# Performance work log

Measured on AMD Instinct MI355X. Metric: run time of the kernel, lower is better.

## Reference

```python
import jax, jax.numpy as jnp
import numpy as np

B, L, C, OUT = 32, 1024, 64, 64
BN_EPS = 1e-5  # PyTorch BatchNorm1d default


def setup_inputs() -> dict:
    key = jax.random.key(0)
    kH, kA, kW = jax.random.split(key, 3)
    H = jax.random.normal(kH, (B, L, C), dtype=jnp.float32)
    A = jax.random.uniform(kA, (B, L, L), dtype=jnp.float32)  # positive degrees
    gamma = jnp.ones((C,), jnp.float32)
    beta = jnp.zeros((C,), jnp.float32)
    W = jax.random.normal(kW, (C, OUT), dtype=jnp.float32) * 0.05
    b = jnp.zeros((OUT,), jnp.float32)
    return {"H": H, "A": A, "gamma": gamma, "beta": beta, "W": W, "b": b}


def reference(H, A, gamma, beta, W, b):
    batch, l, c = H.shape
    # BatchNorm1d in train mode over the flattened (batch*l, c) node axis,
    # biased variance as in PyTorch.
    Hf = H.reshape(batch * l, c)
    mean = Hf.mean(axis=0)
    var = jnp.mean((Hf - mean) ** 2, axis=0)
    Hn = ((Hf - mean) * jax.lax.rsqrt(var + BN_EPS) * gamma + beta).reshape(batch, l, c)
    # Degree normalization: diag(d^0.5) @ A @ diag(d^-0.5) done as row/col scaling
    # (same math as the original's dense diagonal matmuls).
    d = A.sum(axis=2)                                   # [batch, l]
    A_norm = jnp.sqrt(d)[:, :, None] * A * jax.lax.rsqrt(d)[:, None, :]
    A_hat = jnp.eye(l, dtype=A.dtype) - A_norm          # I - D^0.5 A D^-0.5
    # Linear then batched propagation, LeakyReLU (default slope 0.01).
    X = Hn @ W + b                                      # [batch, l, out]
    out = jnp.einsum('bij,bjo->bio', A_hat, X)
    return jax.nn.leaky_relu(out, negative_slope=0.01)
```

## Files before the change

### kernel.cpp

```cpp
#include <hip/hip_runtime.h>

#define NB 32
#define NL 1024
#define NC 64
#define NO 64
constexpr float BN_EPS = 1e-5f;

#define D_OFF 128
#define PART_OFF 32896
#define YT_OFF 131072
#define ABF_OFF 2097152

typedef short          s16x8 __attribute__((ext_vector_type(8)));
typedef unsigned short u16x8 __attribute__((ext_vector_type(8)));
typedef unsigned short u16x4 __attribute__((ext_vector_type(4)));
typedef float          f32x16 __attribute__((ext_vector_type(16)));
typedef float          f32x4  __attribute__((ext_vector_type(4)));

__device__ inline unsigned short f2bf(float f) {
    union { float f; unsigned u; } v; v.f = f;
    unsigned u = v.u + 0x7FFFu + ((v.u >> 16) & 1u);
    return (unsigned short)(u >> 16);
}

__device__ inline void gload16(const void* g, void* l) {
    __builtin_amdgcn_global_load_lds(
        (const __attribute__((address_space(1))) unsigned int*)g,
        (__attribute__((address_space(3))) unsigned int*)l, 16, 0, 0);
}

__global__ __launch_bounds__(256) void degcvt_bn(
    const float* __restrict__ A, const float* __restrict__ H,
    float* __restrict__ ws, unsigned short* __restrict__ Abf) {
    __shared__ f32x4 smem4[2048];
    const int t = threadIdx.x;
    if (blockIdx.x < 1024) {
        const int lane = t & 63, w = t >> 6;
        const size_t row0 = (size_t)blockIdx.x * 32;
        const char* src  = (const char*)A   + row0 * 4096;
        char*       dstA = (char*)Abf       + row0 * 2048;
        const int lo = w * 4096 + lane * 16;
#define STG(bi, c) do {                                                        \
            char* d0 = (char*)(smem4 + (bi) * 1024) + lo;                      \
            const char* s0 = src + (c) * 16384 + lo;                           \
            gload16(s0,        d0);                                            \
            gload16(s0 + 1024, d0 + 1024);                                     \
            gload16(s0 + 2048, d0 + 2048);                                     \
            gload16(s0 + 3072, d0 + 3072);                                     \
        } while (0)
        STG(0, 0);
        __syncthreads();
#pragma unroll 1
        for (int c = 0; c < 8; ++c) {
            if (c + 1 < 8) STG((c + 1) & 1, c + 1);
            const char* cb = (const char*)(smem4 + (c & 1) * 1024) + lo;
            float s = 0.f;
            char* orow = dstA + (size_t)(c * 4 + w) * 2048 + lane * 8;
#pragma unroll
            for (int j = 0; j < 4; ++j) {
                f32x4 v = *(const f32x4*)(cb + j * 1024);
                u16x4 h;
                h[0] = f2bf(v.x); h[1] = f2bf(v.y);
                h[2] = f2bf(v.z); h[3] = f2bf(v.w);
                *(u16x4*)(orow + j * 512) = h;
                s += v.x + v.y + v.z + v.w;
            }
#pragma unroll
            for (int m = 32; m; m >>= 1) s += __shfl_xor(s, m, 64);
            if (lane == 0) ws[D_OFF + row0 + c * 4 + w] = s;
            __syncthreads();
        }
#undef STG
    } else {
        const int bb = blockIdx.x - 1024;
        const float4* Hv = (const float4*)H + bb * 4096;
        float s0 = 0.f, s1 = 0.f, s2 = 0.f, s3 = 0.f;
        float q0 = 0.f, q1 = 0.f, q2 = 0.f, q3 = 0.f;
#pragma unroll 4
        for (int s = 0; s < 16; ++s) {
            float4 v = Hv[s * 256 + t];
            s0 += v.x; q0 += v.x * v.x;
            s1 += v.y; q1 += v.y * v.y;
            s2 += v.z; q2 += v.z * v.z;
            s3 += v.w; q3 += v.w * v.w;
        }
        float* part = (float*)smem4;
        part[t * 8 + 0] = s0; part[t * 8 + 1] = s1;
        part[t * 8 + 2] = s2; part[t * 8 + 3] = s3;
        part[t * 8 + 4] = q0; part[t * 8 + 5] = q1;
        part[t * 8 + 6] = q2; part[t * 8 + 7] = q3;
        __syncthreads();
        if (t < 64) {
            const int g = t >> 2, e = t & 3;
            float a = 0.f, a2 = 0.f;
#pragma unroll
            for (int k = 0; k < 16; ++k) {
                a  += part[(g + 16 * k) * 8 + e];
                a2 += part[(g + 16 * k) * 8 + 4 + e];
            }
            ws[PART_OFF + bb * 64 + t] = a;
            ws[PART_OFF + 128 * 64 + bb * 64 + t] = a2;
        }
    }
}

__global__ __launch_bounds__(256) void linear_xy(
    const float* __restrict__ H, const float* __restrict__ Wm,
    const float* __restrict__ bias, const float* __restrict__ gamma,
    const float* __restrict__ beta, const float* __restrict__ ws,
    float* __restrict__ X, unsigned short* __restrict__ Yt) {
    __shared__ float Wl[NC * NO];
    __shared__ float hnbuf[4][NC];
    __shared__ unsigned short ytile[64][66];
    __shared__ float ls[256], ls2[256];
    __shared__ float sscale[64], sshift[64];
    const int b = blockIdx.x >> 4, ch = blockIdx.x & 15;
    const int r0g = b * NL + ch * 64;
    const int t = threadIdx.x, lane = t & 63, w = t >> 6;
    {
        const float* ps  = ws + PART_OFF;
        const float* ps2 = ws + PART_OFF + 128 * 64;
        const int c = t & 63, q = t >> 6;
        float s = 0.f, s2 = 0.f;
        for (int p = q * 32; p < q * 32 + 32; ++p) {
            s  += ps[p * 64 + c];
            s2 += ps2[p * 64 + c];
        }
        ls[t] = s; ls2[t] = s2;
        __syncthreads();
        if (t < 64) {
            float T  = ls[c]  + ls[c + 64]  + ls[c + 128]  + ls[c + 192];
            float T2 = ls2[c] + ls2[c + 64] + ls2[c + 128] + ls2[c + 192];
            const float n = (float)(NB * NL);
            float mean = T / n;
            float var  = T2 / n - mean * mean;
            float sc = gamma[c] * rsqrtf(var + BN_EPS);
            sscale[c] = sc;
            sshift[c] = beta[c] - mean * sc;
        }
    }
    for (int k = t; k < NC * NO; k += 256) Wl[k] = Wm[k];
    __syncthreads();
    const float sc = sscale[lane];
    const float sh = sshift[lane];
    const float bo = bias[lane];
    const float* dbuf = ws + D_OFF;
    for (int rr = w; rr < 64; rr += 4) {
        const int row = r0g + rr;
        float h = H[(size_t)row * NC + lane];
        hnbuf[w][lane] = h * sc + sh;
        float x = bo;
#pragma unroll
        for (int c4 = 0; c4 < NC; c4 += 4) {
            float4 h4 = *(const float4*)(&hnbuf[w][c4]);
            x += h4.x * Wl[(c4 + 0) * NO + lane];
            x += h4.y * Wl[(c4 + 1) * NO + lane];
            x += h4.z * Wl[(c4 + 2) * NO + lane];
            x += h4.w * Wl[(c4 + 3) * NO + lane];
        }
        X[(size_t)row * NO + lane] = x;
        ytile[rr][lane] = f2bf(x * rsqrtf(dbuf[row]));
    }
    __syncthreads();
    char* ybase = (char*)Yt + (size_t)(b * 16 + ch) * 8192;
#pragma unroll
    for (int i2 = 0; i2 < 16; ++i2) {
        const int col = i2 * 4 + w;
        *(unsigned short*)(ybase + ((col * 128 + lane * 2) ^ ((col & 7) << 4))) =
            ytile[lane][col];
    }
}

__global__ __launch_bounds__(256) void prop_mfma(
    const unsigned short* __restrict__ Abf, const unsigned short* __restrict__ Yt,
    const float* __restrict__ dbuf, float* __restrict__ XO) {

    __shared__ unsigned short Abuf[2][64 * 64];
    __shared__ unsigned short Ybuf[2][64 * 64];
    __shared__ float sdl[64];

    const int b  = blockIdx.x >> 4;
    const int mt = blockIdx.x & 15;
    const int i0 = mt * 64;
    const char* YbT = (const char*)Yt + (size_t)b * 16 * 8192;

    const int t    = threadIdx.x;
    const int lane = t & 63;
    const int w    = t >> 6;

    if (t < 64) sdl[t] = sqrtf(dbuf[b * NL + i0 + t]);

    const int L0  = w * 2048 + lane * 16;
    const int L1  = L0 + 1024;
    const int ar0 = L0 >> 7, ar1 = L1 >> 7;
    const char* Asrc0 = (const char*)Abf
        + ((size_t)(b * NL + i0 + ar0)) * 2048 + ((L0 & 127) ^ ((ar0 & 7) << 4));
    const char* Asrc1 = (const char*)Abf
        + ((size_t)(b * NL + i0 + ar1)) * 2048 + ((L1 & 127) ^ ((ar1 & 7) << 4));

    const int wr0  = (w >> 1) * 32;
    const int wc0  = (w & 1) * 32;
    const int frow = wr0 + (lane & 31);
    const int fcol = wc0 + (lane & 31);
    const int khb  = (lane >> 5) * 16;

    f32x16 acc;
#pragma unroll
    for (int r = 0; r < 16; ++r) acc[r] = 0.f;

#define STAGE(bi, kt) do {                                                     \
        char* adst = (char*)Abuf[bi];                                          \
        gload16(Asrc0 + (size_t)(kt) * 128, adst + L0);                        \
        gload16(Asrc1 + (size_t)(kt) * 128, adst + L1);                        \
        const char* ysrc = YbT + (size_t)(kt) * 8192;                          \
        char* ydst = (char*)Ybuf[bi];                                          \
        gload16(ysrc + L0, ydst + L0);                                         \
        gload16(ysrc + L1, ydst + L1);                                         \
    } while (0)

    STAGE(0, 0);
    __syncthreads();

#pragma unroll 1
    for (int kti = 0; kti < 16; ++kti) {
        const int nxt = kti + 1;
        if (nxt < 16) STAGE(nxt & 1, nxt);
        const char* ab  = (const char*)Abuf[kti & 1];
        const char* yb2 = (const char*)Ybuf[kti & 1];
#pragma unroll
        for (int ks = 0; ks < 4; ++ks) {
            const int kb = ks * 32 + khb;
            s16x8 af = *(const s16x8*)(ab  + ((frow * 128 + kb) ^ ((frow & 7) << 4)));
            s16x8 bf = *(const s16x8*)(yb2 + ((fcol * 128 + kb) ^ ((fcol & 7) << 4)));
            acc = __builtin_amdgcn_mfma_f32_32x32x16_bf16(af, bf, acc, 0, 0, 0);
        }
        __syncthreads();
    }
#undef STAGE

#pragma unroll
    for (int reg = 0; reg < 16; ++reg) {
        int row = (reg & 3) + 8 * (reg >> 2) + 4 * (lane >> 5);
        int i   = i0 + wr0 + row;
        int col = wc0 + (lane & 31);
        size_t idx = ((size_t)(b * NL + i)) * NO + col;
        float x = XO[idx];
        float v = x - sdl[wr0 + row] * acc[reg];
        XO[idx] = v > 0.f ? v : 0.01f * v;
    }
}

extern "C" void kernel_launch(void* const* d_in, const int* in_sizes, int n_in,
                              void* d_out, int out_size, void* d_ws, size_t ws_size,
                              hipStream_t stream) {
    const float* H     = (const float*)d_in[0];
    const float* A     = (const float*)d_in[1];
    const float* gamma = (const float*)d_in[2];
    const float* beta  = (const float*)d_in[3];
    const float* Wm    = (const float*)d_in[4];
    const float* bias  = (const float*)d_in[5];
    float* out = (float*)d_out;
    float* ws  = (float*)d_ws;
    unsigned short* Yt  = (unsigned short*)(ws + YT_OFF);
    unsigned short* Abf = (unsigned short*)(ws + ABF_OFF);

    degcvt_bn<<<1152, 256, 0, stream>>>(A, H, ws, Abf);
    linear_xy<<<512, 256, 0, stream>>>(H, Wm, bias, gamma, beta, ws, out, Yt);
    prop_mfma<<<512, 256, 0, stream>>>(Abf, Yt, ws + D_OFF, out);
}
```

Measured before the change: 69.94 us.

## Drop bf16 copy of A; convert fp32 A to bf16 inside propagation kernel

Removes the bf16 staging copy of the adjacency matrix written by the degree kernel. The propagation kernel now streams fp32 A tiles into LDS and packs them to bf16 with v_cvt_pk_bf16_f32 just before each MFMA. This avoids a large global write and the later bf16 read. In exchange it reads twice as many bytes of A in the matmul, doubles LDS for the A buffers, and adds conversion work in the inner loop.

```diff
diff --git a/kernel.cpp b/kernel.cpp
--- a/kernel.cpp
+++ b/kernel.cpp
@@ -9,11 +9,8 @@
 #define D_OFF 128
 #define PART_OFF 32896
 #define YT_OFF 131072
-#define ABF_OFF 2097152
 
 typedef short          s16x8 __attribute__((ext_vector_type(8)));
-typedef unsigned short u16x8 __attribute__((ext_vector_type(8)));
-typedef unsigned short u16x4 __attribute__((ext_vector_type(4)));
 typedef float          f32x16 __attribute__((ext_vector_type(16)));
 typedef float          f32x4  __attribute__((ext_vector_type(4)));
 
@@ -29,16 +26,24 @@
         (__attribute__((address_space(3))) unsigned int*)l, 16, 0, 0);
 }
 
-__global__ __launch_bounds__(256) void degcvt_bn(
+__device__ inline s16x8 cvt8(f32x4 lo, f32x4 hi) {
+    union { unsigned int i[4]; s16x8 v; } u;
+    asm("v_cvt_pk_bf16_f32 %0, %1, %2" : "=v"(u.i[0]) : "v"(lo.x), "v"(lo.y));
+    asm("v_cvt_pk_bf16_f32 %0, %1, %2" : "=v"(u.i[1]) : "v"(lo.z), "v"(lo.w));
+    asm("v_cvt_pk_bf16_f32 %0, %1, %2" : "=v"(u.i[2]) : "v"(hi.x), "v"(hi.y));
+    asm("v_cvt_pk_bf16_f32 %0, %1, %2" : "=v"(u.i[3]) : "v"(hi.z), "v"(hi.w));
+    return u.v;
+}
+
+__global__ __launch_bounds__(256) void deg_bn(
     const float* __restrict__ A, const float* __restrict__ H,
-    float* __restrict__ ws, unsigned short* __restrict__ Abf) {
+    float* __restrict__ ws) {
     __shared__ f32x4 smem4[2048];
     const int t = threadIdx.x;
     if (blockIdx.x < 1024) {
         const int lane = t & 63, w = t >> 6;
         const size_t row0 = (size_t)blockIdx.x * 32;
-        const char* src  = (const char*)A   + row0 * 4096;
-        char*       dstA = (char*)Abf       + row0 * 2048;
+        const char* src = (const char*)A + row0 * 4096;
         const int lo = w * 4096 + lane * 16;
 #define STG(bi, c) do {                                                        \
             char* d0 = (char*)(smem4 + (bi) * 1024) + lo;                      \
@@ -55,14 +60,9 @@
             if (c + 1 < 8) STG((c + 1) & 1, c + 1);
             const char* cb = (const char*)(smem4 + (c & 1) * 1024) + lo;
             float s = 0.f;
-            char* orow = dstA + (size_t)(c * 4 + w) * 2048 + lane * 8;
 #pragma unroll
             for (int j = 0; j < 4; ++j) {
                 f32x4 v = *(const f32x4*)(cb + j * 1024);
-                u16x4 h;
-                h[0] = f2bf(v.x); h[1] = f2bf(v.y);
-                h[2] = f2bf(v.z); h[3] = f2bf(v.w);
-                *(u16x4*)(orow + j * 512) = h;
                 s += v.x + v.y + v.z + v.w;
             }
 #pragma unroll
@@ -172,17 +172,18 @@
 }
 
 __global__ __launch_bounds__(256) void prop_mfma(
-    const unsigned short* __restrict__ Abf, const unsigned short* __restrict__ Yt,
+    const float* __restrict__ A, const unsigned short* __restrict__ Yt,
     const float* __restrict__ dbuf, float* __restrict__ XO) {
 
-    __shared__ unsigned short Abuf[2][64 * 64];
+    __shared__ float Abuf[2][64 * 64];
     __shared__ unsigned short Ybuf[2][64 * 64];
     __shared__ float sdl[64];
 
     const int b  = blockIdx.x >> 4;
     const int mt = blockIdx.x & 15;
     const int i0 = mt * 64;
-    const char* YbT = (const char*)Yt + (size_t)b * 16 * 8192;
+    const char* Abase = (const char*)A + ((size_t)(b * NL + i0)) * 4096;
+    const char* YbT   = (const char*)Yt + (size_t)b * 16 * 8192;
 
     const int t    = threadIdx.x;
     const int lane = t & 63;
@@ -190,32 +191,39 @@
 
     if (t < 64) sdl[t] = sqrtf(dbuf[b * NL + i0 + t]);
 
-    const int L0  = w * 2048 + lane * 16;
-    const int L1  = L0 + 1024;
-    const int ar0 = L0 >> 7, ar1 = L1 >> 7;
-    const char* Asrc0 = (const char*)Abf
-        + ((size_t)(b * NL + i0 + ar0)) * 2048 + ((L0 & 127) ^ ((ar0 & 7) << 4));
-    const char* Asrc1 = (const char*)Abf
-        + ((size_t)(b * NL + i0 + ar1)) * 2048 + ((L1 & 127) ^ ((ar1 & 7) << 4));
+    const int tr = t >> 4;
+    const int tc = (t & 15) * 16;
+    const char* As[4];
+#pragma unroll
+    for (int i = 0; i < 4; ++i) {
+        const int row = i * 16 + tr;
+        As[i] = Abase + (size_t)row * 4096 + (tc ^ ((row & 7) << 4));
+    }
+    const int yL0 = t * 16, yL1 = t * 16 + 4096;
 
     const int wr0  = (w >> 1) * 32;
     const int wc0  = (w & 1) * 32;
     const int frow = wr0 + (lane & 31);
     const int fcol = wc0 + (lane & 31);
     const int khb  = (lane >> 5) * 16;
+    const int kfh  = (lane >> 5) * 32;
+    const int swA  = (frow & 7) << 4;
+    const int swY  = (fcol & 7) << 4;
 
     f32x16 acc;
 #pragma unroll
     for (int r = 0; r < 16; ++r) acc[r] = 0.f;
 
 #define STAGE(bi, kt) do {                                                     \
-        char* adst = (char*)Abuf[bi];                                          \
-        gload16(Asrc0 + (size_t)(kt) * 128, adst + L0);                        \
-        gload16(Asrc1 + (size_t)(kt) * 128, adst + L1);                        \
-        const char* ysrc = YbT + (size_t)(kt) * 8192;                          \
-        char* ydst = (char*)Ybuf[bi];                                          \
-        gload16(ysrc + L0, ydst + L0);                                         \
-        gload16(ysrc + L1, ydst + L1);                                         \
+        char* ad = (char*)Abuf[bi];                                            \
+        gload16(As[0] + (kt) * 256, ad + t * 16);                              \
+        gload16(As[1] + (kt) * 256, ad + 4096  + t * 16);                      \
+        gload16(As[2] + (kt) * 256, ad + 8192  + t * 16);                      \
+        gload16(As[3] + (kt) * 256, ad + 12288 + t * 16);                      \
+        const char* ys = YbT + (size_t)(kt) * 8192;                            \
+        char* yd = (char*)Ybuf[bi];                                            \
+        gload16(ys + yL0, yd + yL0);                                           \
+        gload16(ys + yL1, yd + yL1);                                           \
     } while (0)
 
     STAGE(0, 0);
@@ -229,9 +237,11 @@
         const char* yb2 = (const char*)Ybuf[kti & 1];
 #pragma unroll
         for (int ks = 0; ks < 4; ++ks) {
-            const int kb = ks * 32 + khb;
-            s16x8 af = *(const s16x8*)(ab  + ((frow * 128 + kb) ^ ((frow & 7) << 4)));
-            s16x8 bf = *(const s16x8*)(yb2 + ((fcol * 128 + kb) ^ ((fcol & 7) << 4)));
+            const int b0 = frow * 256 + ks * 64 + kfh;
+            f32x4 flo = *(const f32x4*)(ab + ((b0)      ^ swA));
+            f32x4 fhi = *(const f32x4*)(ab + ((b0 + 16) ^ swA));
+            s16x8 af = cvt8(flo, fhi);
+            s16x8 bf = *(const s16x8*)(yb2 + ((fcol * 128 + ks * 32 + khb) ^ swY));
             acc = __builtin_amdgcn_mfma_f32_32x32x16_bf16(af, bf, acc, 0, 0, 0);
         }
         __syncthreads();
@@ -261,10 +271,9 @@
     const float* bias  = (const float*)d_in[5];
     float* out = (float*)d_out;
     float* ws  = (float*)d_ws;
-    unsigned short* Yt  = (unsigned short*)(ws + YT_OFF);
-    unsigned short* Abf = (unsigned short*)(ws + ABF_OFF);
-
-    degcvt_bn<<<1152, 256, 0, stream>>>(A, H, ws, Abf);
+    unsigned short* Yt = (unsigned short*)(ws + YT_OFF);
+
+    deg_bn<<<1152, 256, 0, stream>>>(A, H, ws);
     linear_xy<<<512, 256, 0, stream>>>(H, Wm, bias, gamma, beta, ws, out, Yt);
-    prop_mfma<<<512, 256, 0, stream>>>(Abf, Yt, ws + D_OFF, out);
-}
+    prop_mfma<<<512, 256, 0, stream>>>(A, Yt, ws + D_OFF, out);
+}
```

After: 68.65 us. Within noise of the previous version (-1.8%).
